# Optimization experiments

Hardware: AMD Instinct MI355X
Metric: run time of the kernel (lower is better)

## Reference

```python
import jax, jax.numpy as jnp
import numpy as np

N_REFLNS = 2_000_000
N_IMAGES = 8192
N_RAC = 1_000_000
MC = 8
D_META = 16
HIDDEN = 32
LOG_2PI = 1.8378770664093453


def setup_inputs() -> dict:
    key = jax.random.key(0)
    ks = jax.random.split(key, 12)
    return {
        'q_loc': jax.random.normal(ks[0], (N_RAC,), jnp.float32),
        'q_log_scale': 0.1 * jax.random.normal(ks[1], (N_RAC,), jnp.float32) - 1.0,
        'eps': jax.random.normal(ks[2], (MC, N_RAC), jnp.float32),
        'metadata': jax.random.normal(ks[3], (N_REFLNS, D_META), jnp.float32),
        'W1': jax.random.normal(ks[4], (D_META, HIDDEN), jnp.float32) / np.sqrt(D_META),
        'b1': jnp.zeros((HIDDEN,), jnp.float32),
        'W2': jax.random.normal(ks[5], (HIDDEN, MC), jnp.float32) / np.sqrt(HIDDEN),
        'b2': jnp.zeros((MC,), jnp.float32),
        'iobs': jax.random.normal(ks[6], (N_REFLNS,), jnp.float32),
        'sigiobs': jax.random.uniform(ks[7], (N_REFLNS,), jnp.float32) + 0.1,  # positive std
        'image_id': jnp.sort(jax.random.randint(ks[8], (N_REFLNS,), 0, N_IMAGES)),
        'miller_id': jax.random.randint(ks[9], (N_REFLNS,), 0, N_RAC),
    }


def average_by_images(ll, image_id):
    # scatter_add per image, summed over MC samples, then normalized
    per_img = jax.ops.segment_sum(ll.sum(axis=1), image_id, num_segments=N_IMAGES)
    counts = jax.ops.segment_sum(jnp.ones((ll.shape[0],), ll.dtype), image_id, num_segments=N_IMAGES)
    return per_img / jnp.maximum(counts, 1.0) / ll.shape[1]


def reference(q_loc, q_log_scale, eps, metadata, W1, b1, W2, b2, iobs, sigiobs, image_id, miller_id):
    q_scale = jnp.exp(q_log_scale)
    # reparameterized MC samples from surrogate posterior: (MC, N_RAC)
    z = q_loc + q_scale * eps
    # analytic KL( N(loc, scale) || N(0, 1) ) per RAC entry
    kl = 0.5 * (q_scale * q_scale + q_loc * q_loc - 1.0) - q_log_scale
    # scale model: positive per-(refln, sample) scale from metadata
    h = jax.nn.relu(metadata @ W1 + b1)
    scale = jax.nn.softplus(h @ W2 + b2)                # (N_REFLNS, MC)
    # rac.gather: per-reflection structure factor samples
    f = jnp.take(z.T, miller_id, axis=0)                # (N_REFLNS, MC)
    ipred = f * f * scale
    # Normal log-likelihood of iobs given ipred, std sigiobs
    resid = (ipred - iobs[:, None]) / sigiobs[:, None]
    ll = -0.5 * resid * resid - jnp.log(sigiobs)[:, None] - 0.5 * LOG_2PI
    ll_img = average_by_images(ll, image_id)            # (N_IMAGES,)
    ipred_avg = ipred.mean(axis=-1)                     # (N_REFLNS,)
    return ipred_avg, -ll_img.mean(), kl.mean()
```

## Files before the change

### kernel.cpp

```cpp
#include <hip/hip_runtime.h>
#include <math.h>

#define N_REFLNS 2000000
#define N_IMAGES 8192
#define N_RAC    1000000
#define MC       8
#define D_META   16
#define HIDDEN   32
#define LOG_2PI  1.8378770664093453f


__device__ __forceinline__ float softplus_f(float x) {
    return fmaxf(x, 0.0f) + log1pf(expf(-fabsf(x)));
}

__global__ __launch_bounds__(256) void k_z_kl(
    const float* __restrict__ q_loc,
    const float* __restrict__ q_log_scale,
    const float* __restrict__ eps,
    float* __restrict__ zT,
    float* __restrict__ kl_sum)
{
    int r = blockIdx.x * 256 + threadIdx.x;
    float kl = 0.0f;
    if (r < N_RAC) {
        float ql  = q_loc[r];
        float qls = q_log_scale[r];
        float qs  = expf(qls);
        kl = 0.5f * (qs * qs + ql * ql - 1.0f) - qls;
        if (zT) {
            float4 z0, z1;
            z0.x = ql + qs * eps[0 * N_RAC + r];
            z0.y = ql + qs * eps[1 * N_RAC + r];
            z0.z = ql + qs * eps[2 * N_RAC + r];
            z0.w = ql + qs * eps[3 * N_RAC + r];
            z1.x = ql + qs * eps[4 * N_RAC + r];
            z1.y = ql + qs * eps[5 * N_RAC + r];
            z1.z = ql + qs * eps[6 * N_RAC + r];
            z1.w = ql + qs * eps[7 * N_RAC + r];
            float4* dst = (float4*)(zT + (size_t)r * MC);
            dst[0] = z0;
            dst[1] = z1;
        }
    }
    __shared__ float sred[256];
    sred[threadIdx.x] = kl;
    __syncthreads();
    #pragma unroll
    for (int s = 128; s > 0; s >>= 1) {
        if (threadIdx.x < s) sred[threadIdx.x] += sred[threadIdx.x + s];
        __syncthreads();
    }
    if (threadIdx.x == 0) atomicAdd(kl_sum, sred[0]);
}

template <bool HAS_Z>
__global__ __launch_bounds__(256) void k_main(
    const float* __restrict__ metadata,
    const float* __restrict__ W1, const float* __restrict__ b1,
    const float* __restrict__ W2, const float* __restrict__ b2,
    const float* __restrict__ iobs, const float* __restrict__ sigiobs,
    const int* __restrict__ image_id, const int* __restrict__ miller_id,
    const float* __restrict__ zT,
    const float* __restrict__ q_loc, const float* __restrict__ q_log_scale,
    const float* __restrict__ eps,
    float* __restrict__ out_ipred,
    float* __restrict__ img_sum, float* __restrict__ img_cnt)
{
    __shared__ float sW1[D_META * HIDDEN];
    __shared__ float sb1[HIDDEN];
    __shared__ float sW2[HIDDEN * MC];
    __shared__ float sb2[MC];
    __shared__ float s_ll[256];
    __shared__ float s_ct[256];
    __shared__ int   s_id[256];

    int tid = threadIdx.x;
    for (int i = tid; i < D_META * HIDDEN; i += 256) sW1[i] = W1[i];
    if (tid < HIDDEN) sb1[tid] = b1[tid];
    for (int i = tid; i < HIDDEN * MC; i += 256) sW2[i] = W2[i];
    if (tid < MC) sb2[tid] = b2[tid];
    __syncthreads();

    int n = blockIdx.x * 256 + tid;
    bool valid = (n < N_REFLNS);
    float ll_sum = 0.0f;
    int img = -1;

    if (valid) {
        const float4* mrow = (const float4*)(metadata + (size_t)n * D_META);
        float4 m0 = mrow[0], m1 = mrow[1], m2 = mrow[2], m3 = mrow[3];
        float meta[D_META] = {m0.x, m0.y, m0.z, m0.w,
                              m1.x, m1.y, m1.z, m1.w,
                              m2.x, m2.y, m2.z, m2.w,
                              m3.x, m3.y, m3.z, m3.w};
        float acc[MC];
        #pragma unroll
        for (int s = 0; s < MC; s++) acc[s] = sb2[s];
        #pragma unroll
        for (int j = 0; j < HIDDEN; j++) {
            float hj = sb1[j];
            #pragma unroll
            for (int d = 0; d < D_META; d++) hj = fmaf(meta[d], sW1[d * HIDDEN + j], hj);
            hj = fmaxf(hj, 0.0f);
            #pragma unroll
            for (int s = 0; s < MC; s++) acc[s] = fmaf(hj, sW2[j * MC + s], acc[s]);
        }

        int m = miller_id[n];
        float f[MC];
        if (HAS_Z) {
            const float4* zp = (const float4*)(zT + (size_t)m * MC);
            float4 z0 = zp[0], z1 = zp[1];
            f[0] = z0.x; f[1] = z0.y; f[2] = z0.z; f[3] = z0.w;
            f[4] = z1.x; f[5] = z1.y; f[6] = z1.z; f[7] = z1.w;
        } else {
            float ql = q_loc[m];
            float qs = expf(q_log_scale[m]);
            #pragma unroll
            for (int s = 0; s < MC; s++) f[s] = ql + qs * eps[(size_t)s * N_RAC + m];
        }

        float io = iobs[n];
        float sg = sigiobs[n];
        float inv_sg = 1.0f / sg;
        float sum_ip = 0.0f, sum_r2 = 0.0f;
        #pragma unroll
        for (int s = 0; s < MC; s++) {
            float sc = softplus_f(acc[s]);
            float ip = f[s] * f[s] * sc;
            sum_ip += ip;
            float r = (ip - io) * inv_sg;
            sum_r2 = fmaf(r, r, sum_r2);
        }
        out_ipred[n] = sum_ip * (1.0f / MC);
        ll_sum = -0.5f * sum_r2 - (float)MC * (logf(sg) + 0.5f * LOG_2PI);
        img = image_id[n];
    }

    s_ll[tid] = ll_sum;
    s_ct[tid] = valid ? 1.0f : 0.0f;
    s_id[tid] = img;
    __syncthreads();
    #pragma unroll
    for (int d = 1; d < 256; d <<= 1) {
        float a = 0.0f, c = 0.0f;
        if (tid >= d && s_id[tid] == s_id[tid - d]) {
            a = s_ll[tid - d];
            c = s_ct[tid - d];
        }
        __syncthreads();
        s_ll[tid] += a;
        s_ct[tid] += c;
        __syncthreads();
    }
    if (valid) {
        bool tail = (tid == 255) || (s_id[tid + 1] != img);
        if (tail) {
            atomicAdd(&img_sum[img], s_ll[tid]);
            atomicAdd(&img_cnt[img], s_ct[tid]);
        }
    }
}

__global__ __launch_bounds__(256) void k_final(
    const float* __restrict__ img_sum,
    const float* __restrict__ img_cnt,
    const float* __restrict__ kl_sum,
    float* __restrict__ out)
{
    __shared__ float sred[256];
    float acc = 0.0f;
    for (int i = threadIdx.x; i < N_IMAGES; i += 256) {
        acc += img_sum[i] / fmaxf(img_cnt[i], 1.0f);
    }
    sred[threadIdx.x] = acc;
    __syncthreads();
    #pragma unroll
    for (int s = 128; s > 0; s >>= 1) {
        if (threadIdx.x < s) sred[threadIdx.x] += sred[threadIdx.x + s];
        __syncthreads();
    }
    if (threadIdx.x == 0) {
        float mean_ll = sred[0] / ((float)MC * (float)N_IMAGES);
        out[N_REFLNS]     = -mean_ll;
        out[N_REFLNS + 1] = kl_sum[0] * (1.0f / (float)N_RAC);
    }
}

extern "C" void kernel_launch(void* const* d_in, const int* in_sizes, int n_in,
                              void* d_out, int out_size, void* d_ws, size_t ws_size,
                              hipStream_t stream) {
    const float* q_loc       = (const float*)d_in[0];
    const float* q_log_scale = (const float*)d_in[1];
    const float* eps         = (const float*)d_in[2];
    const float* metadata    = (const float*)d_in[3];
    const float* W1          = (const float*)d_in[4];
    const float* b1          = (const float*)d_in[5];
    const float* W2          = (const float*)d_in[6];
    const float* b2          = (const float*)d_in[7];
    const float* iobs        = (const float*)d_in[8];
    const float* sigiobs     = (const float*)d_in[9];
    const int*   image_id    = (const int*)d_in[10];
    const int*   miller_id   = (const int*)d_in[11];
    float* out = (float*)d_out;

    char* ws = (char*)d_ws;
    float* img_sum = (float*)ws;
    float* img_cnt = img_sum + N_IMAGES;
    float* kl_sum  = img_cnt + N_IMAGES;
    const size_t z_off = 65664;
    bool has_z = (ws_size >= z_off + (size_t)N_RAC * MC * sizeof(float));
    float* zT = has_z ? (float*)(ws + z_off) : nullptr;

    hipMemsetAsync(d_ws, 0, (2 * N_IMAGES + 1) * sizeof(float), stream);

    k_z_kl<<<(N_RAC + 255) / 256, 256, 0, stream>>>(q_loc, q_log_scale, eps, zT, kl_sum);

    if (has_z) {
        k_main<true><<<(N_REFLNS + 255) / 256, 256, 0, stream>>>(
            metadata, W1, b1, W2, b2, iobs, sigiobs, image_id, miller_id,
            zT, q_loc, q_log_scale, eps, out, img_sum, img_cnt);
    } else {
        k_main<false><<<(N_REFLNS + 255) / 256, 256, 0, stream>>>(
            metadata, W1, b1, W2, b2, iobs, sigiobs, image_id, miller_id,
            nullptr, q_loc, q_log_scale, eps, out, img_sum, img_cnt);
    }

    k_final<<<1, 256, 0, stream>>>(img_sum, img_cnt, kl_sum, out);
}
```

Measured before the change: 358.1 us.

## Process four reflections per thread with packed weights and vectorized loads

Each thread in the main kernel now handles four consecutive reflections. Every shared-memory weight load is reused across four MLP evaluations, and the per-reflection scalars are read with int4/float4 loads. W1, b1 and W2 are packed into one padded shared array so they can be read as float4, and the z/KL kernel likewise processes four RAC entries per thread with vector loads. The segmented per-image reduction is rebuilt: each thread folds its four entries into head and tail partials and emits atomics for interior segments, then a 512-entry shared scan runs. This raises register pressure, which may lower occupancy, and quarters the number of threads available to hide the random zT gather latency.

```diff
diff --git a/kernel.cpp b/kernel.cpp
--- a/kernel.cpp
+++ b/kernel.cpp
@@ -21,26 +21,35 @@
     float* __restrict__ zT,
     float* __restrict__ kl_sum)
 {
-    int r = blockIdx.x * 256 + threadIdx.x;
+    int t = blockIdx.x * 256 + threadIdx.x;
+    int r0 = t * 4;
     float kl = 0.0f;
-    if (r < N_RAC) {
-        float ql  = q_loc[r];
-        float qls = q_log_scale[r];
-        float qs  = expf(qls);
-        kl = 0.5f * (qs * qs + ql * ql - 1.0f) - qls;
+    if (r0 < N_RAC) {
+        float4 ql  = *(const float4*)(q_loc + r0);
+        float4 qls = *(const float4*)(q_log_scale + r0);
+        float4 qs;
+        qs.x = expf(qls.x); qs.y = expf(qls.y);
+        qs.z = expf(qls.z); qs.w = expf(qls.w);
+        kl = 0.5f * (qs.x * qs.x + ql.x * ql.x - 1.0f) - qls.x
+           + 0.5f * (qs.y * qs.y + ql.y * ql.y - 1.0f) - qls.y
+           + 0.5f * (qs.z * qs.z + ql.z * ql.z - 1.0f) - qls.z
+           + 0.5f * (qs.w * qs.w + ql.w * ql.w - 1.0f) - qls.w;
         if (zT) {
-            float4 z0, z1;
-            z0.x = ql + qs * eps[0 * N_RAC + r];
-            z0.y = ql + qs * eps[1 * N_RAC + r];
-            z0.z = ql + qs * eps[2 * N_RAC + r];
-            z0.w = ql + qs * eps[3 * N_RAC + r];
-            z1.x = ql + qs * eps[4 * N_RAC + r];
-            z1.y = ql + qs * eps[5 * N_RAC + r];
-            z1.z = ql + qs * eps[6 * N_RAC + r];
-            z1.w = ql + qs * eps[7 * N_RAC + r];
-            float4* dst = (float4*)(zT + (size_t)r * MC);
-            dst[0] = z0;
-            dst[1] = z1;
+            float zr[4][MC];
+            #pragma unroll
+            for (int s = 0; s < MC; s++) {
+                float4 e = *(const float4*)(eps + (size_t)s * N_RAC + r0);
+                zr[0][s] = ql.x + qs.x * e.x;
+                zr[1][s] = ql.y + qs.y * e.y;
+                zr[2][s] = ql.z + qs.z * e.z;
+                zr[3][s] = ql.w + qs.w * e.w;
+            }
+            #pragma unroll
+            for (int r = 0; r < 4; r++) {
+                float4* dst = (float4*)(zT + (size_t)(r0 + r) * MC);
+                dst[0] = make_float4(zr[r][0], zr[r][1], zr[r][2], zr[r][3]);
+                dst[1] = make_float4(zr[r][4], zr[r][5], zr[r][6], zr[r][7]);
+            }
         }
     }
     __shared__ float sred[256];
@@ -67,98 +76,159 @@
     float* __restrict__ out_ipred,
     float* __restrict__ img_sum, float* __restrict__ img_cnt)
 {
-    __shared__ float sW1[D_META * HIDDEN];
-    __shared__ float sb1[HIDDEN];
-    __shared__ float sW2[HIDDEN * MC];
+    __shared__ float sW[HIDDEN * 28];
     __shared__ float sb2[MC];
-    __shared__ float s_ll[256];
-    __shared__ float s_ct[256];
-    __shared__ int   s_id[256];
+    __shared__ int   s_id[512];
+    __shared__ float s_ll[512];
+    __shared__ float s_ct[512];
 
     int tid = threadIdx.x;
-    for (int i = tid; i < D_META * HIDDEN; i += 256) sW1[i] = W1[i];
-    if (tid < HIDDEN) sb1[tid] = b1[tid];
-    for (int i = tid; i < HIDDEN * MC; i += 256) sW2[i] = W2[i];
+    for (int idx = tid; idx < HIDDEN * 28; idx += 256) {
+        int j = idx / 28, k = idx % 28;
+        float v = 0.0f;
+        if (k < 16)       v = W1[k * HIDDEN + j];
+        else if (k < 24)  v = W2[j * MC + (k - 16)];
+        else if (k == 24) v = b1[j];
+        sW[idx] = v;
+    }
     if (tid < MC) sb2[tid] = b2[tid];
     __syncthreads();
 
-    int n = blockIdx.x * 256 + tid;
-    bool valid = (n < N_REFLNS);
-    float ll_sum = 0.0f;
-    int img = -1;
+    int n0 = (blockIdx.x * 256 + tid) * 4;
+    bool valid = (n0 < N_REFLNS);
+
+    float ll[4] = {0.f, 0.f, 0.f, 0.f};
+    int   id0 = -1, id1 = -1, id2 = -1, id3 = -1;
+    float c = 0.0f;
 
     if (valid) {
-        const float4* mrow = (const float4*)(metadata + (size_t)n * D_META);
-        float4 m0 = mrow[0], m1 = mrow[1], m2 = mrow[2], m3 = mrow[3];
-        float meta[D_META] = {m0.x, m0.y, m0.z, m0.w,
-                              m1.x, m1.y, m1.z, m1.w,
-                              m2.x, m2.y, m2.z, m2.w,
-                              m3.x, m3.y, m3.z, m3.w};
-        float acc[MC];
+        c = 1.0f;
+        float m[4][D_META];
         #pragma unroll
-        for (int s = 0; s < MC; s++) acc[s] = sb2[s];
+        for (int r = 0; r < 4; r++) {
+            const float4* mrow = (const float4*)(metadata + (size_t)(n0 + r) * D_META);
+            #pragma unroll
+            for (int q = 0; q < 4; q++) {
+                float4 v = mrow[q];
+                m[r][4 * q + 0] = v.x; m[r][4 * q + 1] = v.y;
+                m[r][4 * q + 2] = v.z; m[r][4 * q + 3] = v.w;
+            }
+        }
+
+        float acc[4][MC];
         #pragma unroll
+        for (int r = 0; r < 4; r++)
+            #pragma unroll
+            for (int s = 0; s < MC; s++) acc[r][s] = sb2[s];
+
+        #pragma unroll 4
         for (int j = 0; j < HIDDEN; j++) {
-            float hj = sb1[j];
-            #pragma unroll
-            for (int d = 0; d < D_META; d++) hj = fmaf(meta[d], sW1[d * HIDDEN + j], hj);
-            hj = fmaxf(hj, 0.0f);
-            #pragma unroll
-            for (int s = 0; s < MC; s++) acc[s] = fmaf(hj, sW2[j * MC + s], acc[s]);
-        }
-
-        int m = miller_id[n];
-        float f[MC];
-        if (HAS_Z) {
-            const float4* zp = (const float4*)(zT + (size_t)m * MC);
-            float4 z0 = zp[0], z1 = zp[1];
-            f[0] = z0.x; f[1] = z0.y; f[2] = z0.z; f[3] = z0.w;
-            f[4] = z1.x; f[5] = z1.y; f[6] = z1.z; f[7] = z1.w;
-        } else {
-            float ql = q_loc[m];
-            float qs = expf(q_log_scale[m]);
-            #pragma unroll
-            for (int s = 0; s < MC; s++) f[s] = ql + qs * eps[(size_t)s * N_RAC + m];
-        }
-
-        float io = iobs[n];
-        float sg = sigiobs[n];
-        float inv_sg = 1.0f / sg;
-        float sum_ip = 0.0f, sum_r2 = 0.0f;
+            const float* wr = &sW[j * 28];
+            float4 wa = *(const float4*)(wr + 0);
+            float4 wb = *(const float4*)(wr + 4);
+            float4 wc = *(const float4*)(wr + 8);
+            float4 wd = *(const float4*)(wr + 12);
+            float w1v[D_META] = {wa.x, wa.y, wa.z, wa.w, wb.x, wb.y, wb.z, wb.w,
+                                 wc.x, wc.y, wc.z, wc.w, wd.x, wd.y, wd.z, wd.w};
+            float b1j = wr[24];
+            float h[4];
+            #pragma unroll
+            for (int r = 0; r < 4; r++) {
+                float hr = b1j;
+                #pragma unroll
+                for (int d = 0; d < D_META; d++) hr = fmaf(m[r][d], w1v[d], hr);
+                h[r] = fmaxf(hr, 0.0f);
+            }
+            float4 w2a = *(const float4*)(wr + 16);
+            float4 w2b = *(const float4*)(wr + 20);
+            float w2v[MC] = {w2a.x, w2a.y, w2a.z, w2a.w, w2b.x, w2b.y, w2b.z, w2b.w};
+            #pragma unroll
+            for (int r = 0; r < 4; r++)
+                #pragma unroll
+                for (int s = 0; s < MC; s++) acc[r][s] = fmaf(h[r], w2v[s], acc[r][s]);
+        }
+
+        int4   mi = *(const int4*)(miller_id + n0);
+        float4 io = *(const float4*)(iobs + n0);
+        float4 sg = *(const float4*)(sigiobs + n0);
+        int4   ii = *(const int4*)(image_id + n0);
+        id0 = ii.x; id1 = ii.y; id2 = ii.z; id3 = ii.w;
+        int   mids[4] = {mi.x, mi.y, mi.z, mi.w};
+        float ios[4]  = {io.x, io.y, io.z, io.w};
+        float sgs[4]  = {sg.x, sg.y, sg.z, sg.w};
+        float out4[4];
+
         #pragma unroll
-        for (int s = 0; s < MC; s++) {
-            float sc = softplus_f(acc[s]);
-            float ip = f[s] * f[s] * sc;
-            sum_ip += ip;
-            float r = (ip - io) * inv_sg;
-            sum_r2 = fmaf(r, r, sum_r2);
-        }
-        out_ipred[n] = sum_ip * (1.0f / MC);
-        ll_sum = -0.5f * sum_r2 - (float)MC * (logf(sg) + 0.5f * LOG_2PI);
-        img = image_id[n];
-    }
-
-    s_ll[tid] = ll_sum;
-    s_ct[tid] = valid ? 1.0f : 0.0f;
-    s_id[tid] = img;
+        for (int r = 0; r < 4; r++) {
+            float f[MC];
+            if (HAS_Z) {
+                const float4* zp = (const float4*)(zT + (size_t)mids[r] * MC);
+                float4 z0 = zp[0], z1 = zp[1];
+                f[0] = z0.x; f[1] = z0.y; f[2] = z0.z; f[3] = z0.w;
+                f[4] = z1.x; f[5] = z1.y; f[6] = z1.z; f[7] = z1.w;
+            } else {
+                float qlv = q_loc[mids[r]];
+                float qsv = expf(q_log_scale[mids[r]]);
+                #pragma unroll
+                for (int s = 0; s < MC; s++) f[s] = qlv + qsv * eps[(size_t)s * N_RAC + mids[r]];
+            }
+            float inv_sg = 1.0f / sgs[r];
+            float sum_ip = 0.0f, sum_r2 = 0.0f;
+            #pragma unroll
+            for (int s = 0; s < MC; s++) {
+                float sc = softplus_f(acc[r][s]);
+                float ip = f[s] * f[s] * sc;
+                sum_ip += ip;
+                float rr = (ip - ios[r]) * inv_sg;
+                sum_r2 = fmaf(rr, rr, sum_r2);
+            }
+            out4[r] = sum_ip * (1.0f / MC);
+            ll[r] = -0.5f * sum_r2 - (float)MC * (logf(sgs[r]) + 0.5f * LOG_2PI);
+        }
+        *(float4*)(out_ipred + n0) = make_float4(out4[0], out4[1], out4[2], out4[3]);
+    }
+
+    bool e01 = (id0 == id1), e12 = (id1 == id2), e23 = (id2 == id3);
+    float hll = ll[0], hct = c;
+    if (e01) { hll += ll[1]; hct += c;
+        if (e12) { hll += ll[2]; hct += c;
+            if (e23) { hll += ll[3]; hct += c; } } }
+    bool single = e01 && e12 && e23;
+    int timg; float tll, tct;
+    if (single) { timg = id0; tll = 0.0f; tct = 0.0f; }
+    else {
+        timg = id3; tll = ll[3]; tct = c;
+        if (e23) { tll += ll[2]; tct += c;
+            if (e12) { tll += ll[1]; tct += c; } }
+        bool m1 = !e01 && !(e12 && e23);
+        bool m2 = !(e01 && e12) && !e23;
+        if (m1) { atomicAdd(&img_sum[id1], ll[1]); atomicAdd(&img_cnt[id1], c); }
+        if (m2) { atomicAdd(&img_sum[id2], ll[2]); atomicAdd(&img_cnt[id2], c); }
+    }
+
+    s_id[2 * tid] = id0;  s_ll[2 * tid] = hll;  s_ct[2 * tid] = hct;
+    s_id[2 * tid + 1] = timg; s_ll[2 * tid + 1] = tll; s_ct[2 * tid + 1] = tct;
     __syncthreads();
+
     #pragma unroll
-    for (int d = 1; d < 256; d <<= 1) {
-        float a = 0.0f, c = 0.0f;
-        if (tid >= d && s_id[tid] == s_id[tid - d]) {
-            a = s_ll[tid - d];
-            c = s_ct[tid - d];
-        }
+    for (int d = 1; d < 512; d <<= 1) {
+        int s0 = tid, s1 = tid + 256;
+        float a0 = 0.f, c0 = 0.f, a1 = 0.f, c1 = 0.f;
+        if (s0 >= d && s_id[s0] == s_id[s0 - d]) { a0 = s_ll[s0 - d]; c0 = s_ct[s0 - d]; }
+        if (s1 >= d && s_id[s1] == s_id[s1 - d]) { a1 = s_ll[s1 - d]; c1 = s_ct[s1 - d]; }
         __syncthreads();
-        s_ll[tid] += a;
-        s_ct[tid] += c;
+        s_ll[s0] += a0; s_ct[s0] += c0;
+        s_ll[s1] += a1; s_ct[s1] += c1;
         __syncthreads();
     }
-    if (valid) {
-        bool tail = (tid == 255) || (s_id[tid + 1] != img);
-        if (tail) {
-            atomicAdd(&img_sum[img], s_ll[tid]);
-            atomicAdd(&img_cnt[img], s_ct[tid]);
+
+    #pragma unroll
+    for (int q = 0; q < 2; q++) {
+        int s = tid + q * 256;
+        bool end = (s == 511) || (s_id[s + 1] != s_id[s]);
+        if (end && s_ct[s] > 0.0f) {
+            atomicAdd(&img_sum[s_id[s]], s_ll[s]);
+            atomicAdd(&img_cnt[s_id[s]], s_ct[s]);
         }
     }
 }
@@ -215,14 +285,14 @@
 
     hipMemsetAsync(d_ws, 0, (2 * N_IMAGES + 1) * sizeof(float), stream);
 
-    k_z_kl<<<(N_RAC + 255) / 256, 256, 0, stream>>>(q_loc, q_log_scale, eps, zT, kl_sum);
+    k_z_kl<<<(N_RAC / 4 + 255) / 256, 256, 0, stream>>>(q_loc, q_log_scale, eps, zT, kl_sum);
 
     if (has_z) {
-        k_main<true><<<(N_REFLNS + 255) / 256, 256, 0, stream>>>(
+        k_main<true><<<(N_REFLNS / 4 + 255) / 256, 256, 0, stream>>>(
             metadata, W1, b1, W2, b2, iobs, sigiobs, image_id, miller_id,
             zT, q_loc, q_log_scale, eps, out, img_sum, img_cnt);
     } else {
-        k_main<false><<<(N_REFLNS + 255) / 256, 256, 0, stream>>>(
+        k_main<false><<<(N_REFLNS / 4 + 255) / 256, 256, 0, stream>>>(
             metadata, W1, b1, W2, b2, iobs, sigiobs, image_id, miller_id,
             nullptr, q_loc, q_log_scale, eps, out, img_sum, img_cnt);
     }
```

Result: no change. 351.1 us (-2.0%).
